# Optimization experiments

Measured on AMD Instinct MI355X. Metric: run time of the kernel, lower is better.

The kernel has to match this reference:

```python
import jax, jax.numpy as jnp
import numpy as np
import math

B, N, D, H, FFN = 64, 128, 128, 4, 128
NEG = -9e15
LRELU_SLOPE = 0.2  # LeakyReLU alpha from init_kwargs


def entmax_bisect(x, alpha, n_iter=30):
    # alpha-entmax via bisection (entmax package algorithm); alpha broadcastable, in (1, 2].
    am1 = alpha - 1.0
    x = x * am1
    d = x.shape[-1]
    max_val = jnp.max(x, axis=-1, keepdims=True)
    tau_lo = max_val - 1.0
    tau_hi = max_val - (1.0 / d) ** am1

    def p(tau):
        return jnp.maximum(x - tau, 0.0) ** (1.0 / am1)

    f_lo = jnp.sum(p(tau_lo), axis=-1, keepdims=True) - 1.0
    for _ in range(n_iter):  # fixed iteration count -> jit friendly
        tau_m = 0.5 * (tau_lo + tau_hi)
        f_m = jnp.sum(p(tau_m), axis=-1, keepdims=True) - 1.0
        same = (f_m * f_lo) >= 0
        tau_lo = jnp.where(same, tau_m, tau_lo)
        f_lo = jnp.where(same, f_m, f_lo)
        tau_hi = jnp.where(same, tau_hi, tau_m)
    pm = p(0.5 * (tau_lo + tau_hi))
    return pm / jnp.sum(pm, axis=-1, keepdims=True)


def layernorm(x, g, b, eps=1e-5):
    mu = jnp.mean(x, axis=-1, keepdims=True)
    var = jnp.var(x, axis=-1, keepdims=True)
    return (x - mu) / jnp.sqrt(var + eps) * g + b


def setup_inputs() -> dict:
    key = jax.random.key(0)
    ks = jax.random.split(key, 24)
    s = 0.05
    sw = 1.0 / math.sqrt(D)
    return {
        "hidden": jax.random.normal(ks[0], (B, N, D), jnp.float32),
        "adj": jax.random.randint(ks[1], (B, N, N), 0, 5, jnp.int32),
        "a0": jax.random.normal(ks[2], (D,), jnp.float32) * s,
        "a1": jax.random.normal(ks[3], (D,), jnp.float32) * s,
        "a2": jax.random.normal(ks[4], (D,), jnp.float32) * s,
        "a3": jax.random.normal(ks[5], (D,), jnp.float32) * s,
        "wa": jax.random.normal(ks[6], (D, 1), jnp.float32) * s,
        "ba": jnp.zeros((1,), jnp.float32),
        "wq": jax.random.normal(ks[7], (D, D), jnp.float32) * sw,
        "bq": jnp.zeros((D,), jnp.float32),
        "wk": jax.random.normal(ks[8], (D, D), jnp.float32) * sw,
        "bk": jnp.zeros((D,), jnp.float32),
        "wv": jax.random.normal(ks[9], (D, D), jnp.float32) * sw,
        "bv": jnp.zeros((D,), jnp.float32),
        "w1": jax.random.normal(ks[10], (D, FFN), jnp.float32) * sw,
        "b1": jnp.zeros((FFN,), jnp.float32),
        "w2": jax.random.normal(ks[11], (FFN, D), jnp.float32) * sw,
        "b2": jnp.zeros((D,), jnp.float32),
        "ln_g": jnp.ones((D,), jnp.float32),
        "ln_b": jnp.zeros((D,), jnp.float32),
        "seq_mask": jnp.ones((B, N), jnp.int32),
        "num_heads": H,
    }


def reference(hidden, adj, a0, a1, a2, a3, wa, ba, wq, bq, wk, bk, wv, bv,
              w1, b1, w2, b2, ln_g, ln_b, seq_mask, num_heads):
    Bs, Ns, Ds = hidden.shape
    hd = Ds // num_heads
    # ---- LocalAggregator: relation-typed graph attention (4 edge types) ----
    # e_r[b,i,j] = leakyrelu(sum_d h[b,i,d]*h[b,j,d]*a_r[d]); same math as the
    # original B x N x N x dim repeat/view/matmul, expressed as one contraction.
    A = jnp.stack([a0, a1, a2, a3], axis=1)  # [D, 4]
    e = jax.nn.leaky_relu(jnp.einsum('bid,bjd,dr->bijr', hidden, hidden, A),
                          LRELU_SLOPE)  # [B, N, N, 4]
    att = jnp.full((Bs, Ns, Ns), NEG, dtype=hidden.dtype)
    for r in range(4):  # adj value r+1 selects relation r (original torch.where order)
        att = jnp.where(adj == r + 1, e[..., r], att)
    att = jax.nn.softmax(att, axis=-1)
    local = jnp.einsum('bij,bjd->bid', att, hidden)  # [B, N, D]
    # ---- get_alpha(flag=3): per-session entmax alpha from last position ----
    a_ent = jax.nn.sigmoid(local[:, -1] @ wa + ba) + 1.0  # [B, 1]
    a_ent = jnp.where(a_ent == 1.0, 1.00001, a_ent)
    a_ent = a_ent[:, :, None, None]  # [B,1,1,1] broadcasts over heads/rows/cols
    # ---- EncoderLayer with entmax-bisect multi-head attention (sparse=True) ----
    q = (local @ wq + bq).reshape(Bs, Ns, num_heads, hd).transpose(0, 2, 1, 3)
    k = (local @ wk + bk).reshape(Bs, Ns, num_heads, hd).transpose(0, 2, 1, 3)
    v = (local @ wv + bv).reshape(Bs, Ns, num_heads, hd).transpose(0, 2, 1, 3)
    scores = jnp.einsum('bhid,bhjd->bhij', q, k) / math.sqrt(Ds)  # note: sqrt(dim), as in source
    scores = jnp.where(seq_mask[:, None, None, :] == 0, -1e9, scores)
    alpha = entmax_bisect(scores, a_ent)
    y = jnp.einsum('bhij,bhjd->bhid', alpha, v)
    y = y.transpose(0, 2, 1, 3).reshape(Bs, Ns, Ds)  # output_layer NOT applied (as in source)
    x = local + y
    y2 = jax.nn.relu(y @ w1 + b1) @ w2 + b2  # FFN applied to y, not x (as in source)
    x = x + y2
    return layernorm(x, ln_g, ln_b)
```

## Files before the change

kernel.cpp:

```cpp
#include <hip/hip_runtime.h>
#include <math.h>

#define BB 64
#define NN 128
#define DD 128
#define HH 4
#define HD 32
#define FFN_ 128

static constexpr float NEGV  = -9000000000000000.0f;
static constexpr float SLOPE = 0.2f;
static constexpr float SCALE = 0.08838834764831845f;
#define NEWTON_ITERS 4

__device__ __forceinline__ float4 f4fma(float s, float4 w, float4 a) {
    a.x += s * w.x; a.y += s * w.y; a.z += s * w.z; a.w += s * w.w; return a;
}

__global__ __launch_bounds__(512) void k_att_local(
    const float* __restrict__ hidden, const int* __restrict__ adj,
    const float* __restrict__ a0, const float* __restrict__ a1,
    const float* __restrict__ a2, const float* __restrict__ a3,
    const float* __restrict__ wa, const float* __restrict__ ba,
    float* __restrict__ local, float* __restrict__ aent_out)
{
    __shared__ __align__(16) float At[4][132];
    __shared__ __align__(16) float hb[128][128];
    __shared__ __align__(16) float hA[128][132];
    __shared__ __align__(16) float att[32][132];

    const int blk = blockIdx.x;
    const int b  = blk >> 2;
    const int i0 = (blk & 3) * 32;
    const int tid = threadIdx.x;

    {
        int r = tid >> 7, d = tid & 127;
        float v = (r == 0) ? a0[d] : (r == 1) ? a1[d] : (r == 2) ? a2[d] : a3[d];
        At[r][d] = v;
    }
    #pragma unroll
    for (int p = 0; p < 8; ++p) {
        int q = tid + 512 * p;
        int r = q >> 5, cq = q & 31;
        *reinterpret_cast<float4*>(&hb[r][4 * (cq ^ (r >> 2))]) =
            *reinterpret_cast<const float4*>(&hidden[(size_t)b * NN * DD + (size_t)r * DD + 4 * cq]);
    }
    __syncthreads();

    #pragma unroll
    for (int p = 0; p < 8; ++p) {
        int idx = tid + 512 * p;
        int i  = idx >> 7;
        int r  = (idx >> 5) & 3;
        int dq = idx & 31;
        float4 hv = *reinterpret_cast<const float4*>(&hb[i0 + i][4 * (dq ^ ((i0 + i) >> 2))]);
        float4 av = *reinterpret_cast<const float4*>(&At[r][4 * dq]);
        *reinterpret_cast<float4*>(&hA[i * 4 + r][4 * dq]) =
            make_float4(hv.x * av.x, hv.y * av.y, hv.z * av.z, hv.w * av.w);
    }
    __syncthreads();

    {
        const int ig = tid >> 7;
        const int j  = tid & 127;
        const int ib = 8 * ig;
        const int jx = j >> 2;
        int rowk[8];
        bool vk[8];
        #pragma unroll
        for (int k = 0; k < 8; ++k) {
            int a = adj[(size_t)b * NN * NN + (size_t)(i0 + ib + k) * NN + j];
            bool v = (a >= 1 && a <= 4);
            vk[k] = v;
            rowk[k] = (ib + k) * 4 + (v ? (a - 1) : 0);
        }
        float acc[8];
        #pragma unroll
        for (int k = 0; k < 8; ++k) acc[k] = 0.0f;
        #pragma unroll 2
        for (int dq = 0; dq < 32; ++dq) {
            float4 jv = *reinterpret_cast<const float4*>(&hb[j][4 * (dq ^ jx)]);
            #pragma unroll
            for (int k = 0; k < 8; ++k) {
                float4 A = *reinterpret_cast<const float4*>(&hA[rowk[k]][4 * dq]);
                acc[k] += A.x * jv.x + A.y * jv.y + A.z * jv.z + A.w * jv.w;
            }
        }
        #pragma unroll
        for (int k = 0; k < 8; ++k) {
            float e = (acc[k] > 0.0f) ? acc[k] : SLOPE * acc[k];
            att[ib + k][j] = vk[k] ? e : NEGV;
        }
    }
    __syncthreads();

    const int ti2 = tid >> 5;
    const int tl  = tid & 31;

    #pragma unroll
    for (int rr = 0; rr < 2; ++rr) {
        int row = 2 * ti2 + rr;
        float x0 = att[row][tl], x1 = att[row][tl + 32], x2 = att[row][tl + 64], x3 = att[row][tl + 96];
        float m = fmaxf(fmaxf(x0, x1), fmaxf(x2, x3));
        #pragma unroll
        for (int off = 16; off >= 1; off >>= 1) m = fmaxf(m, __shfl_xor(m, off));
        float q0 = __expf(x0 - m), q1 = __expf(x1 - m), q2 = __expf(x2 - m), q3 = __expf(x3 - m);
        float s = (q0 + q1) + (q2 + q3);
        #pragma unroll
        for (int off = 16; off >= 1; off >>= 1) s += __shfl_xor(s, off);
        float invs = 1.0f / s;
        att[row][tl]      = q0 * invs;
        att[row][tl + 32] = q1 * invs;
        att[row][tl + 64] = q2 * invs;
        att[row][tl + 96] = q3 * invs;
    }

    const int jg = 4 * tl;
    const int rA = 2 * ti2, rB = 2 * ti2 + 1;
    float4 accA = make_float4(0.0f, 0.0f, 0.0f, 0.0f);
    float4 accB = make_float4(0.0f, 0.0f, 0.0f, 0.0f);
    #pragma unroll 4
    for (int jq = 0; jq < 32; ++jq) {
        int xc = 4 * (tl ^ jq);
        #pragma unroll
        for (int k = 0; k < 4; ++k) {
            int j = 4 * jq + k;
            float aAv = att[rA][j];
            float aBv = att[rB][j];
            float4 h4 = *reinterpret_cast<const float4*>(&hb[j][xc]);
            accA.x += aAv * h4.x; accA.y += aAv * h4.y;
            accA.z += aAv * h4.z; accA.w += aAv * h4.w;
            accB.x += aBv * h4.x; accB.y += aBv * h4.y;
            accB.z += aBv * h4.z; accB.w += aBv * h4.w;
        }
    }
    *reinterpret_cast<float4*>(&local[(size_t)b * NN * DD + (size_t)(i0 + rA) * DD + jg]) = accA;
    *reinterpret_cast<float4*>(&local[(size_t)b * NN * DD + (size_t)(i0 + rB) * DD + jg]) = accB;

    if (((blk & 3) == 3) && ti2 == 15) {
        float4 wa4 = *reinterpret_cast<const float4*>(&wa[jg]);
        float dp = accB.x * wa4.x + accB.y * wa4.y + accB.z * wa4.z + accB.w * wa4.w;
        #pragma unroll
        for (int off = 16; off >= 1; off >>= 1) dp += __shfl_xor(dp, off, 32);
        if (tl == 0) {
            float z = dp + ba[0];
            float sig = 1.0f / (1.0f + __expf(-z));
            float a = sig + 1.0f;
            if (a == 1.0f) a = 1.00001f;
            aent_out[b] = a;
        }
    }
}

__global__ __launch_bounds__(1024) void k_qkv_entmax(
    const float* __restrict__ local,
    const float* __restrict__ wq, const float* __restrict__ bq,
    const float* __restrict__ wk, const float* __restrict__ bk,
    const float* __restrict__ wv, const float* __restrict__ bv,
    const float* __restrict__ aent, const int* __restrict__ seq_mask,
    float* __restrict__ y)
{
    __shared__ __align__(16) float lb[128][132];
    __shared__ __align__(16) float wQs[128][36];
    __shared__ __align__(16) float wKs[128][36];
    __shared__ __align__(16) float wVs[128][36];
    __shared__ __align__(16) float kx[32][132];
    __shared__ __align__(16) float vL[128][32];
    __shared__ int maskL[NN];
    __shared__ float aent_sh;

    const int blk = blockIdx.x;
    const int b = blk >> 2, h = blk & 3;
    const int tid = threadIdx.x;

    #pragma unroll
    for (int p = 0; p < 4; ++p) {
        int idx = tid + 1024 * p;
        int r = idx >> 5, cq = idx & 31;
        *reinterpret_cast<float4*>(&lb[r][4 * cq]) =
            *reinterpret_cast<const float4*>(&local[(size_t)b * NN * DD + (size_t)r * DD + 4 * cq]);
    }
    {
        int d = tid >> 3, c4 = 4 * (tid & 7);
        size_t off = (size_t)d * DD + h * HD + c4;
        *reinterpret_cast<float4*>(&wQs[d][c4]) = *reinterpret_cast<const float4*>(&wq[off]);
        *reinterpret_cast<float4*>(&wKs[d][c4]) = *reinterpret_cast<const float4*>(&wk[off]);
        *reinterpret_cast<float4*>(&wVs[d][c4]) = *reinterpret_cast<const float4*>(&wv[off]);
    }
    if (tid < NN) maskL[tid] = seq_mask[b * NN + tid];
    if (tid == 0) aent_sh = aent[b];
    __syncthreads();

    const int t256 = tid & 255;
    const int rp4  = t256 >> 3;
    const int tx4  = t256 & 7;
    const int cg4  = 4 * tx4;
    float4 qa[4];

    if (tid < 256) {
        float4 kb4 = *reinterpret_cast<const float4*>(&bk[h * HD + cg4]);
        float4 vb4 = *reinterpret_cast<const float4*>(&bv[h * HD + cg4]);
        float4 ka0 = kb4, ka1 = kb4, ka2 = kb4, ka3 = kb4;
        float4 va0 = vb4, va1 = vb4, va2 = vb4, va3 = vb4;
        #pragma unroll 4
        for (int kq = 0; kq < 32; ++kq) {
            float4 a0 = *reinterpret_cast<const float4*>(&lb[rp4 +  0][4 * kq]);
            float4 a1 = *reinterpret_cast<const float4*>(&lb[rp4 + 32][4 * kq]);
            float4 a2 = *reinterpret_cast<const float4*>(&lb[rp4 + 64][4 * kq]);
            float4 a3 = *reinterpret_cast<const float4*>(&lb[rp4 + 96][4 * kq]);
            {
                float4 w0 = *reinterpret_cast<const float4*>(&wKs[4 * kq + 0][cg4]);
                float4 w1 = *reinterpret_cast<const float4*>(&wKs[4 * kq + 1][cg4]);
                float4 w2 = *reinterpret_cast<const float4*>(&wKs[4 * kq + 2][cg4]);
                float4 w3 = *reinterpret_cast<const float4*>(&wKs[4 * kq + 3][cg4]);
                ka0 = f4fma(a0.x, w0, ka0); ka0 = f4fma(a0.y, w1, ka0);
                ka0 = f4fma(a0.z, w2, ka0); ka0 = f4fma(a0.w, w3, ka0);
                ka1 = f4fma(a1.x, w0, ka1); ka1 = f4fma(a1.y, w1, ka1);
                ka1 = f4fma(a1.z, w2, ka1); ka1 = f4fma(a1.w, w3, ka1);
                ka2 = f4fma(a2.x, w0, ka2); ka2 = f4fma(a2.y, w1, ka2);
                ka2 = f4fma(a2.z, w2, ka2); ka2 = f4fma(a2.w, w3, ka2);
                ka3 = f4fma(a3.x, w0, ka3); ka3 = f4fma(a3.y, w1, ka3);
                ka3 = f4fma(a3.z, w2, ka3); ka3 = f4fma(a3.w, w3, ka3);
            }
            {
                float4 w0 = *reinterpret_cast<const float4*>(&wVs[4 * kq + 0][cg4]);
                float4 w1 = *reinterpret_cast<const float4*>(&wVs[4 * kq + 1][cg4]);
                float4 w2 = *reinterpret_cast<const float4*>(&wVs[4 * kq + 2][cg4]);
                float4 w3 = *reinterpret_cast<const float4*>(&wVs[4 * kq + 3][cg4]);
                va0 = f4fma(a0.x, w0, va0); va0 = f4fma(a0.y, w1, va0);
                va0 = f4fma(a0.z, w2, va0); va0 = f4fma(a0.w, w3, va0);
                va1 = f4fma(a1.x, w0, va1); va1 = f4fma(a1.y, w1, va1);
                va1 = f4fma(a1.z, w2, va1); va1 = f4fma(a1.w, w3, va1);
                va2 = f4fma(a2.x, w0, va2); va2 = f4fma(a2.y, w1, va2);
                va2 = f4fma(a2.z, w2, va2); va2 = f4fma(a2.w, w3, va2);
                va3 = f4fma(a3.x, w0, va3); va3 = f4fma(a3.y, w1, va3);
                va3 = f4fma(a3.z, w2, va3); va3 = f4fma(a3.w, w3, va3);
            }
        }
        kx[cg4 + 0][rp4 +  0] = ka0.x; kx[cg4 + 1][rp4 +  0] = ka0.y;
        kx[cg4 + 2][rp4 +  0] = ka0.z; kx[cg4 + 3][rp4 +  0] = ka0.w;
        kx[cg4 + 0][rp4 + 32] = ka1.x; kx[cg4 + 1][rp4 + 32] = ka1.y;
        kx[cg4 + 2][rp4 + 32] = ka1.z; kx[cg4 + 3][rp4 + 32] = ka1.w;
        kx[cg4 + 0][rp4 + 64] = ka2.x; kx[cg4 + 1][rp4 + 64] = ka2.y;
        kx[cg4 + 2][rp4 + 64] = ka2.z; kx[cg4 + 3][rp4 + 64] = ka2.w;
        kx[cg4 + 0][rp4 + 96] = ka3.x; kx[cg4 + 1][rp4 + 96] = ka3.y;
        kx[cg4 + 2][rp4 + 96] = ka3.z; kx[cg4 + 3][rp4 + 96] = ka3.w;
        *reinterpret_cast<float4*>(&vL[rp4 +  0][cg4]) = va0;
        *reinterpret_cast<float4*>(&vL[rp4 + 32][cg4]) = va1;
        *reinterpret_cast<float4*>(&vL[rp4 + 64][cg4]) = va2;
        *reinterpret_cast<float4*>(&vL[rp4 + 96][cg4]) = va3;
    } else if (tid < 512) {
        float4 qb4 = *reinterpret_cast<const float4*>(&bq[h * HD + cg4]);
        qa[0] = qb4; qa[1] = qb4; qa[2] = qb4; qa[3] = qb4;
        #pragma unroll 4
        for (int kq = 0; kq < 32; ++kq) {
            float4 a0 = *reinterpret_cast<const float4*>(&lb[rp4 +  0][4 * kq]);
            float4 a1 = *reinterpret_cast<const float4*>(&lb[rp4 + 32][4 * kq]);
            float4 a2 = *reinterpret_cast<const float4*>(&lb[rp4 + 64][4 * kq]);
            float4 a3 = *reinterpret_cast<const float4*>(&lb[rp4 + 96][4 * kq]);
            float4 w0 = *reinterpret_cast<const float4*>(&wQs[4 * kq + 0][cg4]);
            float4 w1 = *reinterpret_cast<const float4*>(&wQs[4 * kq + 1][cg4]);
            float4 w2 = *reinterpret_cast<const float4*>(&wQs[4 * kq + 2][cg4]);
            float4 w3 = *reinterpret_cast<const float4*>(&wQs[4 * kq + 3][cg4]);
            qa[0] = f4fma(a0.x, w0, qa[0]); qa[0] = f4fma(a0.y, w1, qa[0]);
            qa[0] = f4fma(a0.z, w2, qa[0]); qa[0] = f4fma(a0.w, w3, qa[0]);
            qa[1] = f4fma(a1.x, w0, qa[1]); qa[1] = f4fma(a1.y, w1, qa[1]);
            qa[1] = f4fma(a1.z, w2, qa[1]); qa[1] = f4fma(a1.w, w3, qa[1]);
            qa[2] = f4fma(a2.x, w0, qa[2]); qa[2] = f4fma(a2.y, w1, qa[2]);
            qa[2] = f4fma(a2.z, w2, qa[2]); qa[2] = f4fma(a2.w, w3, qa[2]);
            qa[3] = f4fma(a3.x, w0, qa[3]); qa[3] = f4fma(a3.y, w1, qa[3]);
            qa[3] = f4fma(a3.z, w2, qa[3]); qa[3] = f4fma(a3.w, w3, qa[3]);
        }
    }
    __syncthreads();

    if (tid >= 256 && tid < 512) {
        *reinterpret_cast<float4*>(&wQs[rp4 +  0][cg4]) = qa[0];
        *reinterpret_cast<float4*>(&wQs[rp4 + 32][cg4]) = qa[1];
        *reinterpret_cast<float4*>(&wQs[rp4 + 64][cg4]) = qa[2];
        *reinterpret_cast<float4*>(&wQs[rp4 + 96][cg4]) = qa[3];
    }
    __syncthreads();

    if (tid < 512) {
        const int rp  = tid >> 3;
        const int sub = tid & 7;
        const int c0  = 4 * sub;
        const int iA  = rp, iB = rp + 64;

        const float am1 = aent_sh - 1.0f;
        const float inv = 1.0f / am1;
        const float invm1 = inv - 1.0f;
        const float thi_off = exp2f(-7.0f * am1);
        const float sc = SCALE * am1;
        const float xneg = -1000000000.0f * am1;

        float xvA[16], xvB[16];
        #pragma unroll
        for (int s = 0; s < 16; ++s) { xvA[s] = 0.0f; xvB[s] = 0.0f; }
        #pragma unroll
        for (int dq = 0; dq < 8; ++dq) {
            float4 qA = *reinterpret_cast<const float4*>(&wQs[iA][4 * dq]);
            float4 qB = *reinterpret_cast<const float4*>(&wQs[iB][4 * dq]);
            #pragma unroll
            for (int kk = 0; kk < 4; ++kk) {
                int dh = 4 * dq + kk;
                float qa_ = (kk == 0) ? qA.x : (kk == 1) ? qA.y : (kk == 2) ? qA.z : qA.w;
                float qb_ = (kk == 0) ? qB.x : (kk == 1) ? qB.y : (kk == 2) ? qB.z : qB.w;
                #pragma unroll
                for (int qq = 0; qq < 4; ++qq) {
                    float4 k4 = *reinterpret_cast<const float4*>(&kx[dh][c0 + 32 * qq]);
                    xvA[4 * qq + 0] += qa_ * k4.x;  xvB[4 * qq + 0] += qb_ * k4.x;
                    xvA[4 * qq + 1] += qa_ * k4.y;  xvB[4 * qq + 1] += qb_ * k4.y;
                    xvA[4 * qq + 2] += qa_ * k4.z;  xvB[4 * qq + 2] += qb_ * k4.z;
                    xvA[4 * qq + 3] += qa_ * k4.w;  xvB[4 * qq + 3] += qb_ * k4.w;
                }
            }
        }
        #pragma unroll
        for (int qq = 0; qq < 4; ++qq) {
            int4 m4 = *reinterpret_cast<const int4*>(&maskL[c0 + 32 * qq]);
            xvA[4 * qq + 0] = (m4.x == 0) ? xneg : xvA[4 * qq + 0] * sc;
            xvA[4 * qq + 1] = (m4.y == 0) ? xneg : xvA[4 * qq + 1] * sc;
            xvA[4 * qq + 2] = (m4.z == 0) ? xneg : xvA[4 * qq + 2] * sc;
            xvA[4 * qq + 3] = (m4.w == 0) ? xneg : xvA[4 * qq + 3] * sc;
            xvB[4 * qq + 0] = (m4.x == 0) ? xneg : xvB[4 * qq + 0] * sc;
            xvB[4 * qq + 1] = (m4.y == 0) ? xneg : xvB[4 * qq + 1] * sc;
            xvB[4 * qq + 2] = (m4.z == 0) ? xneg : xvB[4 * qq + 2] * sc;
            xvB[4 * qq + 3] = (m4.w == 0) ? xneg : xvB[4 * qq + 3] * sc;
        }

        float mxA = xvA[0], mxB = xvB[0];
        #pragma unroll
        for (int s = 1; s < 16; ++s) { mxA = fmaxf(mxA, xvA[s]); mxB = fmaxf(mxB, xvB[s]); }
        mxA = fmaxf(mxA, __shfl_xor(mxA, 1)); mxB = fmaxf(mxB, __shfl_xor(mxB, 1));
        mxA = fmaxf(mxA, __shfl_xor(mxA, 2)); mxB = fmaxf(mxB, __shfl_xor(mxB, 2));
        mxA = fmaxf(mxA, __shfl_xor(mxA, 4)); mxB = fmaxf(mxB, __shfl_xor(mxB, 4));

        const float hiA = mxA - thi_off, hiB = mxB - thi_off;
        float tauA = mxA - 1.0f, tauB = mxB - 1.0f;

        #pragma unroll
        for (int it = 0; it < NEWTON_ITERS; ++it) {
            float psA = 0.0f, dsA = 0.0f, psB = 0.0f, dsB = 0.0f;
            #pragma unroll
            for (int s = 0; s < 16; ++s) {
                float tA = fmaxf(xvA[s] - tauA, 0.0f);
                float lA = __builtin_amdgcn_logf(tA);
                float dA = __builtin_amdgcn_exp2f(invm1 * lA);
                float pA = tA * dA;
                psA += pA; dsA += dA;
                float tB = fmaxf(xvB[s] - tauB, 0.0f);
                float lB = __builtin_amdgcn_logf(tB);
                float dB = __builtin_amdgcn_exp2f(invm1 * lB);
                float pB = tB * dB;
                psB += pB; dsB += dB;
            }
            psA += __shfl_xor(psA, 1); dsA += __shfl_xor(dsA, 1);
            psA += __shfl_xor(psA, 2); dsA += __shfl_xor(dsA, 2);
            psA += __shfl_xor(psA, 4); dsA += __shfl_xor(dsA, 4);
            psB += __shfl_xor(psB, 1); dsB += __shfl_xor(dsB, 1);
            psB += __shfl_xor(psB, 2); dsB += __shfl_xor(dsB, 2);
            psB += __shfl_xor(psB, 4); dsB += __shfl_xor(dsB, 4);
            tauA = fminf(tauA + (psA - 1.0f) * __builtin_amdgcn_rcpf(inv * dsA), hiA);
            tauB = fminf(tauB + (psB - 1.0f) * __builtin_amdgcn_rcpf(inv * dsB), hiB);
        }

        {
            float pm[16]; float S = 0.0f;
            #pragma unroll
            for (int s = 0; s < 16; ++s) {
                float t = fmaxf(xvA[s] - tauA, 0.0f);
                float l = __builtin_amdgcn_logf(t);
                float p = t * __builtin_amdgcn_exp2f(invm1 * l);
                pm[s] = p; S += p;
            }
            S += __shfl_xor(S, 1); S += __shfl_xor(S, 2); S += __shfl_xor(S, 4);
            float invS = __builtin_amdgcn_rcpf(S);
            #pragma unroll
            for (int qq = 0; qq < 4; ++qq) {
                float4 a4 = make_float4(pm[4 * qq + 0] * invS, pm[4 * qq + 1] * invS,
                                        pm[4 * qq + 2] * invS, pm[4 * qq + 3] * invS);
                *reinterpret_cast<float4*>(&lb[iA][c0 + 32 * qq]) = a4;
            }
        }
        {
            float pm[16]; float S = 0.0f;
            #pragma unroll
            for (int s = 0; s < 16; ++s) {
                float t = fmaxf(xvB[s] - tauB, 0.0f);
                float l = __builtin_amdgcn_logf(t);
                float p = t * __builtin_amdgcn_exp2f(invm1 * l);
                pm[s] = p; S += p;
            }
            S += __shfl_xor(S, 1); S += __shfl_xor(S, 2); S += __shfl_xor(S, 4);
            float invS = __builtin_amdgcn_rcpf(S);
            #pragma unroll
            for (int qq = 0; qq < 4; ++qq) {
                float4 a4 = make_float4(pm[4 * qq + 0] * invS, pm[4 * qq + 1] * invS,
                                        pm[4 * qq + 2] * invS, pm[4 * qq + 3] * invS);
                *reinterpret_cast<float4*>(&lb[iB][c0 + 32 * qq]) = a4;
            }
        }

        float4 accA = make_float4(0.0f, 0.0f, 0.0f, 0.0f);
        float4 accB = make_float4(0.0f, 0.0f, 0.0f, 0.0f);
        #pragma unroll 4
        for (int q2 = 0; q2 < 32; ++q2) {
            float4 aA = *reinterpret_cast<const float4*>(&lb[iA][4 * q2]);
            float4 aB = *reinterpret_cast<const float4*>(&lb[iB][4 * q2]);
            float4 v0 = *reinterpret_cast<const float4*>(&vL[4 * q2 + 0][c0]);
            float4 v1 = *reinterpret_cast<const float4*>(&vL[4 * q2 + 1][c0]);
            float4 v2 = *reinterpret_cast<const float4*>(&vL[4 * q2 + 2][c0]);
            float4 v3 = *reinterpret_cast<const float4*>(&vL[4 * q2 + 3][c0]);
            accA.x += aA.x * v0.x + aA.y * v1.x + aA.z * v2.x + aA.w * v3.x;
            accA.y += aA.x * v0.y + aA.y * v1.y + aA.z * v2.y + aA.w * v3.y;
            accA.z += aA.x * v0.z + aA.y * v1.z + aA.z * v2.z + aA.w * v3.z;
            accA.w += aA.x * v0.w + aA.y * v1.w + aA.z * v2.w + aA.w * v3.w;
            accB.x += aB.x * v0.x + aB.y * v1.x + aB.z * v2.x + aB.w * v3.x;
            accB.y += aB.x * v0.y + aB.y * v1.y + aB.z * v2.y + aB.w * v3.y;
            accB.z += aB.x * v0.z + aB.y * v1.z + aB.z * v2.z + aB.w * v3.z;
            accB.w += aB.x * v0.w + aB.y * v1.w + aB.z * v2.w + aB.w * v3.w;
        }
        *reinterpret_cast<float4*>(&y[(size_t)b * NN * DD + (size_t)iA * DD + h * HD + c0]) = accA;
        *reinterpret_cast<float4*>(&y[(size_t)b * NN * DD + (size_t)iB * DD + h * HD + c0]) = accB;
    }
}

__global__ __launch_bounds__(512) void k_ffn_ln(
    const float* __restrict__ yv, const float* __restrict__ w1,
    const float* __restrict__ b1, const float* __restrict__ w2,
    const float* __restrict__ b2, const float* __restrict__ local,
    const float* __restrict__ g, const float* __restrict__ bb,
    float* __restrict__ out)
{
    __shared__ __align__(16) float Bs[128][128];
    __shared__ __align__(16) float As[32][128];
    const int mt = blockIdx.x;
    const int b  = mt >> 2;
    const int i0 = (mt & 3) * 32;
    const int tid = threadIdx.x;

    #pragma unroll
    for (int p = 0; p < 8; ++p) {
        int idx = tid + 512 * p;
        int d = idx >> 5, cq = idx & 31;
        *reinterpret_cast<float4*>(&Bs[d][4 * cq]) =
            *reinterpret_cast<const float4*>(&w1[d * FFN_ + 4 * cq]);
    }
    #pragma unroll
    for (int p = 0; p < 2; ++p) {
        int idx = tid + 512 * p;
        int row = idx >> 5, kq = idx & 31;
        *reinterpret_cast<float4*>(&As[row][4 * kq]) =
            *reinterpret_cast<const float4*>(&yv[(size_t)b * NN * DD + (size_t)(i0 + row) * DD + 4 * kq]);
    }
    __syncthreads();

    const int tx = tid & 31, ty = tid >> 5;
    const int c0 = 4 * tx;

    {
        float4 bias = *reinterpret_cast<const float4*>(&b1[c0]);
        float acc[2][4];
        #pragma unroll
        for (int i = 0; i < 2; ++i)
            #pragma unroll
            for (int j = 0; j < 4; ++j) acc[i][j] = 0.0f;
        #pragma unroll 2
        for (int kq = 0; kq < 32; ++kq) {
            float4 b0 = *reinterpret_cast<const float4*>(&Bs[4 * kq + 0][c0]);
            float4 b1v = *reinterpret_cast<const float4*>(&Bs[4 * kq + 1][c0]);
            float4 b2v = *reinterpret_cast<const float4*>(&Bs[4 * kq + 2][c0]);
            float4 b3v = *reinterpret_cast<const float4*>(&Bs[4 * kq + 3][c0]);
            #pragma unroll
            for (int i = 0; i < 2; ++i) {
                float4 a = *reinterpret_cast<const float4*>(&As[2 * ty + i][4 * kq]);
                acc[i][0] += a.x * b0.x + a.y * b1v.x + a.z * b2v.x + a.w * b3v.x;
                acc[i][1] += a.x * b0.y + a.y * b1v.y + a.z * b2v.y + a.w * b3v.y;
                acc[i][2] += a.x * b0.z + a.y * b1v.z + a.z * b2v.z + a.w * b3v.z;
                acc[i][3] += a.x * b0.w + a.y * b1v.w + a.z * b2v.w + a.w * b3v.w;
            }
        }
        #pragma unroll
        for (int i = 0; i < 2; ++i) {
            *reinterpret_cast<float4*>(&As[2 * ty + i][c0]) =
                make_float4(fmaxf(acc[i][0] + bias.x, 0.0f), fmaxf(acc[i][1] + bias.y, 0.0f),
                            fmaxf(acc[i][2] + bias.z, 0.0f), fmaxf(acc[i][3] + bias.w, 0.0f));
        }
    }
    __syncthreads();

    #pragma unroll
    for (int p = 0; p < 8; ++p) {
        int idx = tid + 512 * p;
        int d = idx >> 5, cq = idx & 31;
        *reinterpret_cast<float4*>(&Bs[d][4 * cq]) =
            *reinterpret_cast<const float4*>(&w2[d * DD + 4 * cq]);
    }
    __syncthreads();

    float4 bias = *reinterpret_cast<const float4*>(&b2[c0]);
    float4 g4 = *reinterpret_cast<const float4*>(&g[c0]);
    float4 bb4 = *reinterpret_cast<const float4*>(&bb[c0]);
    float acc[2][4];
    #pragma unroll
    for (int i = 0; i < 2; ++i)
        #pragma unroll
        for (int j = 0; j < 4; ++j) acc[i][j] = 0.0f;
    #pragma unroll 2
    for (int kq = 0; kq < 32; ++kq) {
        float4 b0 = *reinterpret_cast<const float4*>(&Bs[4 * kq + 0][c0]);
        float4 b1v = *reinterpret_cast<const float4*>(&Bs[4 * kq + 1][c0]);
        float4 b2v = *reinterpret_cast<const float4*>(&Bs[4 * kq + 2][c0]);
        float4 b3v = *reinterpret_cast<const float4*>(&Bs[4 * kq + 3][c0]);
        #pragma unroll
        for (int i = 0; i < 2; ++i) {
            float4 a = *reinterpret_cast<const float4*>(&As[2 * ty + i][4 * kq]);
            acc[i][0] += a.x * b0.x + a.y * b1v.x + a.z * b2v.x + a.w * b3v.x;
            acc[i][1] += a.x * b0.y + a.y * b1v.y + a.z * b2v.y + a.w * b3v.y;
            acc[i][2] += a.x * b0.z + a.y * b1v.z + a.z * b2v.z + a.w * b3v.z;
            acc[i][3] += a.x * b0.w + a.y * b1v.w + a.z * b2v.w + a.w * b3v.w;
        }
    }

    #pragma unroll
    for (int i = 0; i < 2; ++i) {
        size_t base = (size_t)b * NN * DD + (size_t)(i0 + 2 * ty + i) * DD + c0;
        float4 l4 = *reinterpret_cast<const float4*>(&local[base]);
        float4 y4 = *reinterpret_cast<const float4*>(&yv[base]);
        float x0 = acc[i][0] + bias.x + l4.x + y4.x;
        float x1 = acc[i][1] + bias.y + l4.y + y4.y;
        float x2 = acc[i][2] + bias.z + l4.z + y4.z;
        float x3 = acc[i][3] + bias.w + l4.w + y4.w;

        float s = (x0 + x1) + (x2 + x3);
        s += __shfl_xor(s, 1); s += __shfl_xor(s, 2); s += __shfl_xor(s, 4);
        s += __shfl_xor(s, 8); s += __shfl_xor(s, 16);
        float mu = s * (1.0f / 128.0f);
        float d0 = x0 - mu, d1 = x1 - mu, d2 = x2 - mu, d3 = x3 - mu;
        float v = (d0 * d0 + d1 * d1) + (d2 * d2 + d3 * d3);
        v += __shfl_xor(v, 1); v += __shfl_xor(v, 2); v += __shfl_xor(v, 4);
        v += __shfl_xor(v, 8); v += __shfl_xor(v, 16);
        float rstd = rsqrtf(v * (1.0f / 128.0f) + 1e-5f);
        float4 o = make_float4(d0 * rstd * g4.x + bb4.x, d1 * rstd * g4.y + bb4.y,
                               d2 * rstd * g4.z + bb4.z, d3 * rstd * g4.w + bb4.w);
        *reinterpret_cast<float4*>(&out[base]) = o;
    }
}

extern "C" void kernel_launch(void* const* d_in, const int* in_sizes, int n_in,
                              void* d_out, int out_size, void* d_ws, size_t ws_size,
                              hipStream_t stream) {
    const float* hidden = (const float*)d_in[0];
    const int*   adj    = (const int*)d_in[1];
    const float* a0 = (const float*)d_in[2];
    const float* a1 = (const float*)d_in[3];
    const float* a2 = (const float*)d_in[4];
    const float* a3 = (const float*)d_in[5];
    const float* wa = (const float*)d_in[6];
    const float* ba = (const float*)d_in[7];
    const float* wq = (const float*)d_in[8];
    const float* bq = (const float*)d_in[9];
    const float* wk = (const float*)d_in[10];
    const float* bk = (const float*)d_in[11];
    const float* wv = (const float*)d_in[12];
    const float* bv = (const float*)d_in[13];
    const float* w1 = (const float*)d_in[14];
    const float* b1 = (const float*)d_in[15];
    const float* w2 = (const float*)d_in[16];
    const float* b2 = (const float*)d_in[17];
    const float* g  = (const float*)d_in[18];
    const float* bb = (const float*)d_in[19];
    const int* seq_mask = (const int*)d_in[20];

    float* ws   = (float*)d_ws;
    float* local = ws;
    float* yv    = ws + 1048576;
    float* aentw = ws + 2 * 1048576;
    float* out   = (float*)d_out;

    k_att_local<<<dim3(256), dim3(512), 0, stream>>>(hidden, adj, a0, a1, a2, a3,
                                                     wa, ba, local, aentw);
    k_qkv_entmax<<<dim3(256), dim3(1024), 0, stream>>>(local, wq, bq, wk, bk, wv, bv,
                                                       aentw, seq_mask, yv);
    k_ffn_ln<<<dim3(256), dim3(512), 0, stream>>>(yv, w1, b1, w2, b2, local, g, bb, out);
}
```

Baseline: 65.65 us.

## Spread Q/K/V projection across all 1024 threads with two rows each

The QKV projection previously used only 512 threads (256 computing K and V, 256 computing Q), each handling four rows. It now uses all 1024 threads: 512 compute K/V and 512 compute Q, each handling two rows. This halves the serial work per thread and the accumulator register pressure, at the cost of loading each weight vector from shared memory twice as often. It assumes a block size of 1024, which the existing load loop using tid+1024*p already implies.

```diff
diff --git a/kernel.cpp b/kernel.cpp
--- a/kernel.cpp
+++ b/kernel.cpp
@@ -192,100 +192,75 @@
     if (tid == 0) aent_sh = aent[b];
     __syncthreads();
 
-    const int t256 = tid & 255;
-    const int rp4  = t256 >> 3;
-    const int tx4  = t256 & 7;
-    const int cg4  = 4 * tx4;
-    float4 qa[4];
-
-    if (tid < 256) {
-        float4 kb4 = *reinterpret_cast<const float4*>(&bk[h * HD + cg4]);
-        float4 vb4 = *reinterpret_cast<const float4*>(&bv[h * HD + cg4]);
-        float4 ka0 = kb4, ka1 = kb4, ka2 = kb4, ka3 = kb4;
-        float4 va0 = vb4, va1 = vb4, va2 = vb4, va3 = vb4;
+    const int t512 = tid & 511;
+    const int rp   = t512 >> 3;
+    const int txg  = t512 & 7;
+    const int cg   = 4 * txg;
+    const int r0 = rp, r1 = rp + 64;
+    float4 qa0, qa1;
+
+    if (tid < 512) {
+        float4 kb4 = *reinterpret_cast<const float4*>(&bk[h * HD + cg]);
+        float4 vb4 = *reinterpret_cast<const float4*>(&bv[h * HD + cg]);
+        float4 ka0 = kb4, ka1 = kb4, va0 = vb4, va1 = vb4;
         #pragma unroll 4
         for (int kq = 0; kq < 32; ++kq) {
-            float4 a0 = *reinterpret_cast<const float4*>(&lb[rp4 +  0][4 * kq]);
-            float4 a1 = *reinterpret_cast<const float4*>(&lb[rp4 + 32][4 * kq]);
-            float4 a2 = *reinterpret_cast<const float4*>(&lb[rp4 + 64][4 * kq]);
-            float4 a3 = *reinterpret_cast<const float4*>(&lb[rp4 + 96][4 * kq]);
+            float4 a0 = *reinterpret_cast<const float4*>(&lb[r0][4 * kq]);
+            float4 a1 = *reinterpret_cast<const float4*>(&lb[r1][4 * kq]);
             {
-                float4 w0 = *reinterpret_cast<const float4*>(&wKs[4 * kq + 0][cg4]);
-                float4 w1 = *reinterpret_cast<const float4*>(&wKs[4 * kq + 1][cg4]);
-                float4 w2 = *reinterpret_cast<const float4*>(&wKs[4 * kq + 2][cg4]);
-                float4 w3 = *reinterpret_cast<const float4*>(&wKs[4 * kq + 3][cg4]);
+                float4 w0 = *reinterpret_cast<const float4*>(&wKs[4 * kq + 0][cg]);
+                float4 w1 = *reinterpret_cast<const float4*>(&wKs[4 * kq + 1][cg]);
+                float4 w2 = *reinterpret_cast<const float4*>(&wKs[4 * kq + 2][cg]);
+                float4 w3 = *reinterpret_cast<const float4*>(&wKs[4 * kq + 3][cg]);
                 ka0 = f4fma(a0.x, w0, ka0); ka0 = f4fma(a0.y, w1, ka0);
                 ka0 = f4fma(a0.z, w2, ka0); ka0 = f4fma(a0.w, w3, ka0);
                 ka1 = f4fma(a1.x, w0, ka1); ka1 = f4fma(a1.y, w1, ka1);
                 ka1 = f4fma(a1.z, w2, ka1); ka1 = f4fma(a1.w, w3, ka1);
-                ka2 = f4fma(a2.x, w0, ka2); ka2 = f4fma(a2.y, w1, ka2);
-                ka2 = f4fma(a2.z, w2, ka2); ka2 = f4fma(a2.w, w3, ka2);
-                ka3 = f4fma(a3.x, w0, ka3); ka3 = f4fma(a3.y, w1, ka3);
-                ka3 = f4fma(a3.z, w2, ka3); ka3 = f4fma(a3.w, w3, ka3);
             }
             {
-                float4 w0 = *reinterpret_cast<const float4*>(&wVs[4 * kq + 0][cg4]);
-                float4 w1 = *reinterpret_cast<const float4*>(&wVs[4 * kq + 1][cg4]);
-                float4 w2 = *reinterpret_cast<const float4*>(&wVs[4 * kq + 2][cg4]);
-                float4 w3 = *reinterpret_cast<const float4*>(&wVs[4 * kq + 3][cg4]);
+                float4 w0 = *reinterpret_cast<const float4*>(&wVs[4 * kq + 0][cg]);
+                float4 w1 = *reinterpret_cast<const float4*>(&wVs[4 * kq + 1][cg]);
+                float4 w2 = *reinterpret_cast<const float4*>(&wVs[4 * kq + 2][cg]);
+                float4 w3 = *reinterpret_cast<const float4*>(&wVs[4 * kq + 3][cg]);
                 va0 = f4fma(a0.x, w0, va0); va0 = f4fma(a0.y, w1, va0);
                 va0 = f4fma(a0.z, w2, va0); va0 = f4fma(a0.w, w3, va0);
                 va1 = f4fma(a1.x, w0, va1); va1 = f4fma(a1.y, w1, va1);
                 va1 = f4fma(a1.z, w2, va1); va1 = f4fma(a1.w, w3, va1);
-                va2 = f4fma(a2.x, w0, va2); va2 = f4fma(a2.y, w1, va2);
-                va2 = f4fma(a2.z, w2, va2); va2 = f4fma(a2.w, w3, va2);
-                va3 = f4fma(a3.x, w0, va3); va3 = f4fma(a3.y, w1, va3);
-                va3 = f4fma(a3.z, w2, va3); va3 = f4fma(a3.w, w3, va3);
-            }
-        }
-        kx[cg4 + 0][rp4 +  0] = ka0.x; kx[cg4 + 1][rp4 +  0] = ka0.y;
-        kx[cg4 + 2][rp4 +  0] = ka0.z; kx[cg4 + 3][rp4 +  0] = ka0.w;
-        kx[cg4 + 0][rp4 + 32] = ka1.x; kx[cg4 + 1][rp4 + 32] = ka1.y;
-        kx[cg4 + 2][rp4 + 32] = ka1.z; kx[cg4 + 3][rp4 + 32] = ka1.w;
-        kx[cg4 + 0][rp4 + 64] = ka2.x; kx[cg4 + 1][rp4 + 64] = ka2.y;
-        kx[cg4 + 2][rp4 + 64] = ka2.z; kx[cg4 + 3][rp4 + 64] = ka2.w;
-        kx[cg4 + 0][rp4 + 96] = ka3.x; kx[cg4 + 1][rp4 + 96] = ka3.y;
-        kx[cg4 + 2][rp4 + 96] = ka3.z; kx[cg4 + 3][rp4 + 96] = ka3.w;
-        *reinterpret_cast<float4*>(&vL[rp4 +  0][cg4]) = va0;
-        *reinterpret_cast<float4*>(&vL[rp4 + 32][cg4]) = va1;
-        *reinterpret_cast<float4*>(&vL[rp4 + 64][cg4]) = va2;
-        *reinterpret_cast<float4*>(&vL[rp4 + 96][cg4]) = va3;
-    } else if (tid < 512) {
-        float4 qb4 = *reinterpret_cast<const float4*>(&bq[h * HD + cg4]);
-        qa[0] = qb4; qa[1] = qb4; qa[2] = qb4; qa[3] = qb4;
+            }
+        }
+        kx[cg + 0][r0] = ka0.x; kx[cg + 1][r0] = ka0.y;
+        kx[cg + 2][r0] = ka0.z; kx[cg + 3][r0] = ka0.w;
+        kx[cg + 0][r1] = ka1.x; kx[cg + 1][r1] = ka1.y;
+        kx[cg + 2][r1] = ka1.z; kx[cg + 3][r1] = ka1.w;
+        *reinterpret_cast<float4*>(&vL[r0][cg]) = va0;
+        *reinterpret_cast<float4*>(&vL[r1][cg]) = va1;
+    } else {
+        float4 qb4 = *reinterpret_cast<const float4*>(&bq[h * HD + cg]);
+        qa0 = qb4; qa1 = qb4;
         #pragma unroll 4
         for (int kq = 0; kq < 32; ++kq) {
-            float4 a0 = *reinterpret_cast<const float4*>(&lb[rp4 +  0][4 * kq]);
-            float4 a1 = *reinterpret_cast<const float4*>(&lb[rp4 + 32][4 * kq]);
-            float4 a2 = *reinterpret_cast<const float4*>(&lb[rp4 + 64][4 * kq]);
-            float4 a3 = *reinterpret_cast<const float4*>(&lb[rp4 + 96][4 * kq]);
-            float4 w0 = *reinterpret_cast<const float4*>(&wQs[4 * kq + 0][cg4]);
-            float4 w1 = *reinterpret_cast<const float4*>(&wQs[4 * kq + 1][cg4]);
-            float4 w2 = *reinterpret_cast<const float4*>(&wQs[4 * kq + 2][cg4]);
-            float4 w3 = *reinterpret_cast<const float4*>(&wQs[4 * kq + 3][cg4]);
-            qa[0] = f4fma(a0.x, w0, qa[0]); qa[0] = f4fma(a0.y, w1, qa[0]);
-            qa[0] = f4fma(a0.z, w2, qa[0]); qa[0] = f4fma(a0.w, w3, qa[0]);
-            qa[1] = f4fma(a1.x, w0, qa[1]); qa[1] = f4fma(a1.y, w1, qa[1]);
-            qa[1] = f4fma(a1.z, w2, qa[1]); qa[1] = f4fma(a1.w, w3, qa[1]);
-            qa[2] = f4fma(a2.x, w0, qa[2]); qa[2] = f4fma(a2.y, w1, qa[2]);
-            qa[2] = f4fma(a2.z, w2, qa[2]); qa[2] = f4fma(a2.w, w3, qa[2]);
-            qa[3] = f4fma(a3.x, w0, qa[3]); qa[3] = f4fma(a3.y, w1, qa[3]);
-            qa[3] = f4fma(a3.z, w2, qa[3]); qa[3] = f4fma(a3.w, w3, qa[3]);
-        }
-    }
-    __syncthreads();
-
-    if (tid >= 256 && tid < 512) {
-        *reinterpret_cast<float4*>(&wQs[rp4 +  0][cg4]) = qa[0];
-        *reinterpret_cast<float4*>(&wQs[rp4 + 32][cg4]) = qa[1];
-        *reinterpret_cast<float4*>(&wQs[rp4 + 64][cg4]) = qa[2];
-        *reinterpret_cast<float4*>(&wQs[rp4 + 96][cg4]) = qa[3];
+            float4 a0 = *reinterpret_cast<const float4*>(&lb[r0][4 * kq]);
+            float4 a1 = *reinterpret_cast<const float4*>(&lb[r1][4 * kq]);
+            float4 w0 = *reinterpret_cast<const float4*>(&wQs[4 * kq + 0][cg]);
+            float4 w1 = *reinterpret_cast<const float4*>(&wQs[4 * kq + 1][cg]);
+            float4 w2 = *reinterpret_cast<const float4*>(&wQs[4 * kq + 2][cg]);
+            float4 w3 = *reinterpret_cast<const float4*>(&wQs[4 * kq + 3][cg]);
+            qa0 = f4fma(a0.x, w0, qa0); qa0 = f4fma(a0.y, w1, qa0);
+            qa0 = f4fma(a0.z, w2, qa0); qa0 = f4fma(a0.w, w3, qa0);
+            qa1 = f4fma(a1.x, w0, qa1); qa1 = f4fma(a1.y, w1, qa1);
+            qa1 = f4fma(a1.z, w2, qa1); qa1 = f4fma(a1.w, w3, qa1);
+        }
+    }
+    __syncthreads();
+
+    if (tid >= 512) {
+        *reinterpret_cast<float4*>(&wQs[r0][cg]) = qa0;
+        *reinterpret_cast<float4*>(&wQs[r1][cg]) = qa1;
     }
     __syncthreads();
 
     if (tid < 512) {
-        const int rp  = tid >> 3;
-        const int sub = tid & 7;
+        const int sub = t512 & 7;
         const int c0  = 4 * sub;
         const int iA  = rp, iB = rp + 64;
 
```

After: 65.09 us, median of 2. About the same (-0.8%).
